# Kernel tuning notes

Measured on AMD Instinct MI355X. Metric: run time of the kernel, lower is better.

The kernel has to match this reference:

```python
import jax, jax.numpy as jnp
import numpy as np

# LightGCN propagation constants
N_USERS = 50000
N_ITEMS = 100000
N_NODES = N_USERS + N_ITEMS          # rows of the symmetric normalized adjacency
N_EDGES = 2400000                    # nnz of sparse adjacency (avg degree ~16)
LATENT_DIM = 64                      # config['latent_dim_rec']
N_LAYERS = 3                         # config['lightGCN_n_layers']
BATCH = 4096


def setup_inputs() -> dict:
    key = jax.random.key(0)
    ks = jax.random.split(key, 7)
    # Embedding tables, init std=0.1 as in nn.init.normal_(std=0.1)
    emb_user = 0.1 * jax.random.normal(ks[0], (N_USERS, LATENT_DIM), dtype=jnp.float32)
    emb_item = 0.1 * jax.random.normal(ks[1], (N_ITEMS, LATENT_DIM), dtype=jnp.float32)
    # Sparse normalized adjacency in COO form (fixed structure reused every layer)
    src = jax.random.randint(ks[2], (N_EDGES,), 0, N_NODES, dtype=jnp.int32)
    dst = jax.random.randint(ks[3], (N_EDGES,), 0, N_NODES, dtype=jnp.int32)
    # values ~ 1/sqrt(deg_i * deg_j) scale for avg degree 16
    vals = jax.random.uniform(ks[4], (N_EDGES,), dtype=jnp.float32) / 16.0
    users = jax.random.randint(ks[5], (BATCH,), 0, N_USERS, dtype=jnp.int32)
    items = jax.random.randint(ks[6], (BATCH,), 0, N_ITEMS, dtype=jnp.int32)
    return {"emb_user": emb_user, "emb_item": emb_item, "vals": vals,
            "src": src, "dst": dst, "users": users, "items": items}


def _spmm(vals, src, dst, x):
    # y[dst] += vals * x[src]  == torch.sparse.mm(G, x)
    return jax.ops.segment_sum(vals[:, None] * x[src], dst, num_segments=N_NODES)


def reference(emb_user, emb_item, vals, src, dst, users, items):
    # computer(): stack layer embeddings and mean-pool, fused as running sum
    all_emb = jnp.concatenate([emb_user, emb_item], axis=0)  # [N, D]
    acc = all_emb
    x = all_emb
    for _ in range(N_LAYERS):
        x = _spmm(vals, src, dst, x)
        acc = acc + x
    light_out = acc / jnp.asarray(N_LAYERS + 1, dtype=acc.dtype)
    users_emb = light_out[users]                 # [B, D]
    items_emb = light_out[N_USERS + items]       # [B, D]
    gamma = jnp.sum(users_emb * items_emb, axis=1)  # [B]
    return gamma
```

## Files before the change

### kernel.cpp

```cpp
#include <hip/hip_runtime.h>


#define N_USERS 50000
#define N_ITEMS 100000
#define N_NODES 150000
#define N_EDGES 2400000
#define DIM 64
#define BATCH 4096

#define CHUNKS 512
#define CHUNK_EDGES 4688
#define PPT 5
#define KB 256
#define NPB 586
#define ECAP 10240
#define GSTR 16
#define CONVB 2344

typedef unsigned int uint;
typedef float v2f __attribute__((ext_vector_type(2)));

__device__ __forceinline__ uint pack_bf16(float a, float b) {
    uint ua = __float_as_uint(a), ub = __float_as_uint(b);
    ua = (ua + 0x7FFFu + ((ua >> 16) & 1u)) >> 16;
    ub = (ub + 0x7FFFu + ((ub >> 16) & 1u)) >> 16;
    return ua | (ub << 16);
}

__device__ __forceinline__ v2f unpack_bf16x2(uint w) {
    v2f r;
    r.x = __uint_as_float(w << 16);
    r.y = __uint_as_float(w & 0xFFFF0000u);
    return r;
}

__global__ __launch_bounds__(1024) void part_kernel(
        const int* __restrict__ src, const int* __restrict__ dstA,
        const float* __restrict__ vals, int* __restrict__ gcur,
        int2* __restrict__ coarse,
        const float* __restrict__ emb_user, const float* __restrict__ emb_item,
        uint2* __restrict__ t0) {
    int t = threadIdx.x;
    if (blockIdx.x >= CHUNKS) {
        int i = (blockIdx.x - CHUNKS) * 1024 + t;
        if (i < N_NODES * DIM / 4) {
            const int userN4 = N_USERS * DIM / 4;
            float4 v;
            if (i < userN4) v = ((const float4*)emb_user)[i];
            else            v = ((const float4*)emb_item)[i - userN4];
            t0[i] = make_uint2(pack_bf16(v.x, v.y), pack_bf16(v.z, v.w));
        }
        return;
    }
    __shared__ int2 stage[CHUNK_EDGES];
    __shared__ unsigned char stage_b[CHUNK_EDGES];
    __shared__ int h[KB];
    __shared__ int hoff[KB];
    __shared__ int delta[KB];
    __shared__ int wsum4[4];
    int c = blockIdx.x;
    if (t < KB) h[t] = 0;
    __syncthreads();
    int base = c * CHUNK_EDGES;
    int ecnt = min(CHUNK_EDGES, N_EDGES - base);
    int d_c[PPT];
    int r_c[PPT];
#pragma unroll
    for (int u = 0; u < PPT; ++u) {
        int i = t + u * 1024;
        d_c[u] = 0;
        r_c[u] = 0;
        if (i < ecnt) {
            int d = dstA[base + i];
            d_c[u] = d;
            r_c[u] = atomicAdd(&h[(int)((unsigned)d / NPB)], 1);
        }
    }
    __syncthreads();
    int lane = t & 63, wid = t >> 6;
    if (t < KB) {
        int v = h[t];
        int incl = v;
#pragma unroll
        for (int o = 1; o < 64; o <<= 1) {
            int add = __shfl_up(incl, o, 64);
            if (lane >= o) incl += add;
        }
        hoff[t] = incl - v;
        if (lane == 63) wsum4[wid] = incl;
    }
    __syncthreads();
    if (t < 64) {
        int vv = (lane < 4) ? wsum4[lane] : 0;
        int inc2 = vv;
#pragma unroll
        for (int o = 1; o < 4; o <<= 1) {
            int add = __shfl_up(inc2, o, 64);
            if (lane >= o) inc2 += add;
        }
        if (lane < 4) wsum4[lane] = inc2 - vv;
    }
    __syncthreads();
    if (t < KB) {
        int off = hoff[t] + wsum4[t >> 6];
        hoff[t] = off;
        int cb = atomicAdd(&gcur[t * GSTR], h[t]);
        delta[t] = t * ECAP + cb - off;
    }
    __syncthreads();
#pragma unroll
    for (int u = 0; u < PPT; ++u) {
        int i = t + u * 1024;
        if (i < ecnt) {
            int e = base + i;
            int d = d_c[u];
            int b = (int)((unsigned)d / NPB);
            int dl = d - b * NPB;
            int pos = hoff[b] + r_c[u];
            stage[pos] = make_int2(src[e] | (dl << 18), __float_as_int(vals[e]));
            stage_b[pos] = (unsigned char)b;
        }
    }
    __syncthreads();
#pragma unroll
    for (int u = 0; u < PPT; ++u) {
        int j = t + u * 1024;
        if (j < ecnt) {
            int b = stage_b[j];
            int idx = j + delta[b];
            if (idx < (b + 1) * ECAP)
                coarse[idx] = stage[j];
        }
    }
}

__global__ __launch_bounds__(1024) void p4f_fine(int2* __restrict__ coarse,
                                                 const int* __restrict__ gcur,
                                                 uint* __restrict__ rowinfo) {
    __shared__ int2 eds[ECAP];
    __shared__ unsigned short iperm[ECAP];
    __shared__ int cnt[640];
    __shared__ int rs_[640];
    __shared__ int cur_[640];
    __shared__ int wsum[16];
    int k = blockIdx.x, t = threadIdx.x;
    int rbase = k * ECAP;
    int ne = min(gcur[k * GSTR], ECAP);
    for (int i = t; i < ne; i += 1024) eds[i] = coarse[rbase + i];
    if (t < 640) cnt[t] = 0;
    __syncthreads();
    for (int i = t; i < ne; i += 1024)
        atomicAdd(&cnt[eds[i].x >> 18], 1);
    __syncthreads();
    int wid = t >> 6, lane = t & 63;
    if (t < 640) {
        int v = cnt[t];
        int incl = v;
#pragma unroll
        for (int o = 1; o < 64; o <<= 1) {
            int add = __shfl_up(incl, o, 64);
            if (lane >= o) incl += add;
        }
        rs_[t] = incl - v;
        if (lane == 63) wsum[wid] = incl;
    }
    __syncthreads();
    if (t < 64) {
        int vv = (lane < 10) ? wsum[lane] : 0;
        int inc2 = vv;
#pragma unroll
        for (int o = 1; o < 16; o <<= 1) {
            int add = __shfl_up(inc2, o, 64);
            if (lane >= o) inc2 += add;
        }
        if (lane < 10) wsum[lane] = inc2 - vv;
    }
    __syncthreads();
    if (t < 640) rs_[t] += wsum[wid];
    __syncthreads();
    int nodes0 = k * NPB;
    int nb = min(NPB, N_NODES - nodes0);
    if (t < nb)
        rowinfo[nodes0 + t] = (uint)(rbase + rs_[t]) | ((uint)cnt[t] << 22);
    if (t < 640) cur_[t] = rs_[t];
    __syncthreads();
    for (int i = t; i < ne; i += 1024) {
        int dl = eds[i].x >> 18;
        int p = atomicAdd(&cur_[dl], 1);
        iperm[p] = (unsigned short)i;
    }
    __syncthreads();
    for (int j = t; j < ne; j += 1024) {
        int2 ev = eds[iperm[j]];
        coarse[rbase + j] = make_int2(ev.x & 0x3FFFF, ev.y);
    }
}

__global__ __launch_bounds__(256) void spmm_kernel(
        const uint* __restrict__ rowinfo, const int2* __restrict__ epair,
        const uint* __restrict__ xin, uint* __restrict__ xout) {
    int wave = (blockIdx.x * 256 + threadIdx.x) >> 6;
    int lane = threadIdx.x & 63;
    int g = lane >> 3;
    int l = lane & 7;
    int n = wave * 8 + g;
    bool live = n < N_NODES;
    uint ri = live ? rowinfo[n] : 0u;
    int s = (int)(ri & 0x3FFFFFu);
    int e = live ? s + (int)(ri >> 22) : s;
    int gbase = g * 8;
    v2f a0 = {0.f, 0.f}, a1 = {0.f, 0.f}, a2 = {0.f, 0.f}, a3 = {0.f, 0.f};
    for (int jb = s; jb < e; jb += 8) {
        int jl = jb + l;
        int2 ev = epair[jl < e ? jl : (e - 1)];
        float vw = (jl < e) ? __int_as_float(ev.y) : 0.f;
        int sx = ev.x;
        int srcs[8];
        float ws[8];
#pragma unroll
        for (int u = 0; u < 8; ++u) {
            srcs[u] = __shfl(sx, gbase + u, 64);
            ws[u]   = __shfl(vw, gbase + u, 64);
        }
        uint4 r[8];
#pragma unroll
        for (int u = 0; u < 8; ++u)
            r[u] = ((const uint4*)(xin + (size_t)srcs[u] * 32))[l];
#pragma unroll
        for (int u = 0; u < 8; ++u) {
            a0 += ws[u] * unpack_bf16x2(r[u].x);
            a1 += ws[u] * unpack_bf16x2(r[u].y);
            a2 += ws[u] * unpack_bf16x2(r[u].z);
            a3 += ws[u] * unpack_bf16x2(r[u].w);
        }
    }
    if (live) {
        uint4 o;
        o.x = pack_bf16(a0.x, a0.y);
        o.y = pack_bf16(a1.x, a1.y);
        o.z = pack_bf16(a2.x, a2.y);
        o.w = pack_bf16(a3.x, a3.y);
        ((uint4*)(xout + (size_t)n * 32))[l] = o;
    }
}

__global__ __launch_bounds__(256) void batch_row_kernel(
        const int* __restrict__ users, const int* __restrict__ items,
        const float* __restrict__ emb_user, const float* __restrict__ emb_item,
        const uint* __restrict__ x1, const uint* __restrict__ x2,
        const uint* __restrict__ rowinfo, const int2* __restrict__ epair,
        float4* __restrict__ rows) {
    int w = (blockIdx.x * 256 + threadIdx.x) >> 6;
    int lane = threadIdx.x & 63;
    int g = lane >> 4;
    int l = lane & 15;
    bool isU = w < BATCH;
    int b = isU ? w : w - BATCH;
    int idx = isU ? users[b] : items[b];
    int n = isU ? idx : N_USERS + idx;
    uint ri = rowinfo[n];
    int s = (int)(ri & 0x3FFFFFu);
    int e = s + (int)(ri >> 22);
    v2f a0 = {0.f, 0.f}, a1 = {0.f, 0.f};
    for (int j0 = s + g; j0 < e; j0 += 16) {
        int2 ev[4];
        float vv[4];
        uint2 rr[4];
#pragma unroll
        for (int u = 0; u < 4; ++u) {
            int j = j0 + 4 * u;
            bool p = (u == 0) || (j < e);
            ev[u] = epair[p ? j : j0];
            vv[u] = p ? __int_as_float(ev[u].y) : 0.f;
        }
#pragma unroll
        for (int u = 0; u < 4; ++u)
            rr[u] = ((const uint2*)(x2 + (size_t)ev[u].x * 32))[l];
#pragma unroll
        for (int u = 0; u < 4; ++u) {
            a0 += vv[u] * unpack_bf16x2(rr[u].x);
            a1 += vv[u] * unpack_bf16x2(rr[u].y);
        }
    }
#pragma unroll
    for (int off = 16; off < 64; off <<= 1) {
        a0.x += __shfl_xor(a0.x, off, 64);
        a0.y += __shfl_xor(a0.y, off, 64);
        a1.x += __shfl_xor(a1.x, off, 64);
        a1.y += __shfl_xor(a1.y, off, 64);
    }
    if (g == 0) {
        const float* t0row = isU ? (emb_user + (size_t)idx * DIM)
                                 : (emb_item + (size_t)idx * DIM);
        float4 x0 = ((const float4*)t0row)[l];
        uint2 w1 = ((const uint2*)(x1 + (size_t)n * 32))[l];
        uint2 w2 = ((const uint2*)(x2 + (size_t)n * 32))[l];
        v2f b10 = unpack_bf16x2(w1.x), b11 = unpack_bf16x2(w1.y);
        v2f b20 = unpack_bf16x2(w2.x), b21 = unpack_bf16x2(w2.y);
        float4 r;
        r.x = x0.x + b10.x + b20.x + a0.x;
        r.y = x0.y + b10.y + b20.y + a0.y;
        r.z = x0.z + b11.x + b21.x + a1.x;
        r.w = x0.w + b11.y + b21.y + a1.y;
        rows[(size_t)w * 16 + l] = r;
    }
}

__global__ __launch_bounds__(256) void dot_kernel(const float* __restrict__ rows,
                                                  float* __restrict__ out) {
    int t = blockIdx.x * 256 + threadIdx.x;
    int b = t >> 6;
    int lane = t & 63;
    float p = rows[(size_t)b * DIM + lane] * rows[(size_t)(BATCH + b) * DIM + lane];
#pragma unroll
    for (int o = 32; o > 0; o >>= 1) p += __shfl_down(p, o, 64);
    if (lane == 0) out[b] = p * (1.0f / 16.0f);
}

extern "C" void kernel_launch(void* const* d_in, const int* in_sizes, int n_in,
                              void* d_out, int out_size, void* d_ws, size_t ws_size,
                              hipStream_t stream) {
    const float* emb_user = (const float*)d_in[0];
    const float* emb_item = (const float*)d_in[1];
    const float* vals     = (const float*)d_in[2];
    const int*   src      = (const int*)d_in[3];
    const int*   dst      = (const int*)d_in[4];
    const int*   users    = (const int*)d_in[5];
    const int*   items    = (const int*)d_in[6];
    float* out = (float*)d_out;

    char* ws = (char*)d_ws;
    size_t off = 0;
    auto walloc = [&](size_t bytes) -> void* {
        void* p = ws + off;
        off += (bytes + 255) & ~(size_t)255;
        return p;
    };
    const size_t ROWB = (size_t)N_NODES * DIM * 2;
    uint* t0          = (uint*)walloc(ROWB);
    uint* x1          = (uint*)walloc(ROWB);
    uint* x2          = (uint*)walloc(ROWB);
    int2* coarse      = (int2*)walloc((size_t)KB * ECAP * 8);
    int*  gcur        = (int*) walloc((size_t)KB * GSTR * 4);
    uint* rowinfo     = (uint*)walloc((size_t)N_NODES * 4);
    float4* rows      = (float4*)walloc((size_t)2 * BATCH * DIM * 4);

    hipMemsetAsync(gcur, 0, (size_t)KB * GSTR * 4, stream);

    part_kernel<<<CHUNKS + CONVB, 1024, 0, stream>>>(
        src, dst, vals, gcur, coarse, emb_user, emb_item, (uint2*)t0);
    p4f_fine<<<KB, 1024, 0, stream>>>(coarse, gcur, rowinfo);

    const int SPMM_BLOCKS = (N_NODES / 8 * 64 + 255) / 256;
    spmm_kernel<<<SPMM_BLOCKS, 256, 0, stream>>>(rowinfo, coarse, t0, x1);
    spmm_kernel<<<SPMM_BLOCKS, 256, 0, stream>>>(rowinfo, coarse, x1, x2);
    batch_row_kernel<<<(2 * BATCH) / 4, 256, 0, stream>>>(
        users, items, emb_user, emb_item, x1, x2, rowinfo, coarse, rows);
    dot_kernel<<<(BATCH * 64) / 256, 256, 0, stream>>>((const float*)rows, out);
}
```

Before: 236.0 us.

## Fuse batch row gather with dot product and reuse counting atomics for bucketing

The final layer's per-row gather and the dot-product kernel become one kernel. Each wave handles one batch pair, user row in the lower half and item row in the upper half, and the halves are combined with cross-lane shuffles. This removes the intermediate rows buffer and one launch. Separately, the fine partition kernel keeps the atomicAdd return values from the counting pass as within-bucket offsets, which drops the second atomic pass and one barrier. The cost is that each row now gets half as many lanes for its edge loop, and the atomic results must sit in registers.

```diff
diff --git a/kernel.cpp b/kernel.cpp
--- a/kernel.cpp
+++ b/kernel.cpp
@@ -14,6 +14,7 @@
 #define KB 256
 #define NPB 586
 #define ECAP 10240
+#define MAXIT 10
 #define GSTR 16
 #define CONVB 2344
 
@@ -141,7 +142,6 @@
     __shared__ unsigned short iperm[ECAP];
     __shared__ int cnt[640];
     __shared__ int rs_[640];
-    __shared__ int cur_[640];
     __shared__ int wsum[16];
     int k = blockIdx.x, t = threadIdx.x;
     int rbase = k * ECAP;
@@ -149,8 +149,14 @@
     for (int i = t; i < ne; i += 1024) eds[i] = coarse[rbase + i];
     if (t < 640) cnt[t] = 0;
     __syncthreads();
-    for (int i = t; i < ne; i += 1024)
-        atomicAdd(&cnt[eds[i].x >> 18], 1);
+    int rr[MAXIT];
+#pragma unroll
+    for (int u = 0; u < MAXIT; ++u) {
+        int i = t + u * 1024;
+        rr[u] = 0;
+        if (i < ne)
+            rr[u] = atomicAdd(&cnt[eds[i].x >> 18], 1);
+    }
     __syncthreads();
     int wid = t >> 6, lane = t & 63;
     if (t < 640) {
@@ -182,12 +188,13 @@
     int nb = min(NPB, N_NODES - nodes0);
     if (t < nb)
         rowinfo[nodes0 + t] = (uint)(rbase + rs_[t]) | ((uint)cnt[t] << 22);
-    if (t < 640) cur_[t] = rs_[t];
-    __syncthreads();
-    for (int i = t; i < ne; i += 1024) {
-        int dl = eds[i].x >> 18;
-        int p = atomicAdd(&cur_[dl], 1);
-        iperm[p] = (unsigned short)i;
+#pragma unroll
+    for (int u = 0; u < MAXIT; ++u) {
+        int i = t + u * 1024;
+        if (i < ne) {
+            int dl = eds[i].x >> 18;
+            iperm[rs_[dl] + rr[u]] = (unsigned short)i;
+        }
     }
     __syncthreads();
     for (int j = t; j < ne; j += 1024) {
@@ -244,31 +251,30 @@
     }
 }
 
-__global__ __launch_bounds__(256) void batch_row_kernel(
+__global__ __launch_bounds__(256) void batch_dot_kernel(
         const int* __restrict__ users, const int* __restrict__ items,
         const float* __restrict__ emb_user, const float* __restrict__ emb_item,
         const uint* __restrict__ x1, const uint* __restrict__ x2,
         const uint* __restrict__ rowinfo, const int2* __restrict__ epair,
-        float4* __restrict__ rows) {
-    int w = (blockIdx.x * 256 + threadIdx.x) >> 6;
+        float* __restrict__ out) {
+    int b = (blockIdx.x * 256 + threadIdx.x) >> 6;
     int lane = threadIdx.x & 63;
-    int g = lane >> 4;
+    int hg = (lane >> 4) & 1;
     int l = lane & 15;
-    bool isU = w < BATCH;
-    int b = isU ? w : w - BATCH;
+    bool isU = lane < 32;
     int idx = isU ? users[b] : items[b];
     int n = isU ? idx : N_USERS + idx;
     uint ri = rowinfo[n];
     int s = (int)(ri & 0x3FFFFFu);
     int e = s + (int)(ri >> 22);
     v2f a0 = {0.f, 0.f}, a1 = {0.f, 0.f};
-    for (int j0 = s + g; j0 < e; j0 += 16) {
+    for (int j0 = s + hg; j0 < e; j0 += 8) {
         int2 ev[4];
         float vv[4];
         uint2 rr[4];
 #pragma unroll
         for (int u = 0; u < 4; ++u) {
-            int j = j0 + 4 * u;
+            int j = j0 + 2 * u;
             bool p = (u == 0) || (j < e);
             ev[u] = epair[p ? j : j0];
             vv[u] = p ? __int_as_float(ev[u].y) : 0.f;
@@ -282,38 +288,28 @@
             a1 += vv[u] * unpack_bf16x2(rr[u].y);
         }
     }
-#pragma unroll
-    for (int off = 16; off < 64; off <<= 1) {
-        a0.x += __shfl_xor(a0.x, off, 64);
-        a0.y += __shfl_xor(a0.y, off, 64);
-        a1.x += __shfl_xor(a1.x, off, 64);
-        a1.y += __shfl_xor(a1.y, off, 64);
-    }
-    if (g == 0) {
-        const float* t0row = isU ? (emb_user + (size_t)idx * DIM)
-                                 : (emb_item + (size_t)idx * DIM);
-        float4 x0 = ((const float4*)t0row)[l];
-        uint2 w1 = ((const uint2*)(x1 + (size_t)n * 32))[l];
-        uint2 w2 = ((const uint2*)(x2 + (size_t)n * 32))[l];
-        v2f b10 = unpack_bf16x2(w1.x), b11 = unpack_bf16x2(w1.y);
-        v2f b20 = unpack_bf16x2(w2.x), b21 = unpack_bf16x2(w2.y);
-        float4 r;
-        r.x = x0.x + b10.x + b20.x + a0.x;
-        r.y = x0.y + b10.y + b20.y + a0.y;
-        r.z = x0.z + b11.x + b21.x + a1.x;
-        r.w = x0.w + b11.y + b21.y + a1.y;
-        rows[(size_t)w * 16 + l] = r;
-    }
-}
-
-__global__ __launch_bounds__(256) void dot_kernel(const float* __restrict__ rows,
-                                                  float* __restrict__ out) {
-    int t = blockIdx.x * 256 + threadIdx.x;
-    int b = t >> 6;
-    int lane = t & 63;
-    float p = rows[(size_t)b * DIM + lane] * rows[(size_t)(BATCH + b) * DIM + lane];
-#pragma unroll
-    for (int o = 32; o > 0; o >>= 1) p += __shfl_down(p, o, 64);
+    a0.x += __shfl_xor(a0.x, 16, 64);
+    a0.y += __shfl_xor(a0.y, 16, 64);
+    a1.x += __shfl_xor(a1.x, 16, 64);
+    a1.y += __shfl_xor(a1.y, 16, 64);
+    const float* t0row = isU ? (emb_user + (size_t)idx * DIM)
+                             : (emb_item + (size_t)idx * DIM);
+    float4 x0 = ((const float4*)t0row)[l];
+    uint2 w1 = ((const uint2*)(x1 + (size_t)n * 32))[l];
+    uint2 w2 = ((const uint2*)(x2 + (size_t)n * 32))[l];
+    v2f b10 = unpack_bf16x2(w1.x), b11 = unpack_bf16x2(w1.y);
+    v2f b20 = unpack_bf16x2(w2.x), b21 = unpack_bf16x2(w2.y);
+    float rx = x0.x + b10.x + b20.x + a0.x;
+    float ry = x0.y + b10.y + b20.y + a0.y;
+    float rz = x0.z + b11.x + b21.x + a1.x;
+    float rw = x0.w + b11.y + b21.y + a1.y;
+    float ox = __shfl_xor(rx, 32, 64);
+    float oy = __shfl_xor(ry, 32, 64);
+    float oz = __shfl_xor(rz, 32, 64);
+    float ow = __shfl_xor(rw, 32, 64);
+    float p = rx * ox + ry * oy + rz * oz + rw * ow;
+#pragma unroll
+    for (int o = 1; o < 16; o <<= 1) p += __shfl_xor(p, o, 64);
     if (lane == 0) out[b] = p * (1.0f / 16.0f);
 }
 
@@ -343,7 +339,6 @@
     int2* coarse      = (int2*)walloc((size_t)KB * ECAP * 8);
     int*  gcur        = (int*) walloc((size_t)KB * GSTR * 4);
     uint* rowinfo     = (uint*)walloc((size_t)N_NODES * 4);
-    float4* rows      = (float4*)walloc((size_t)2 * BATCH * DIM * 4);
 
     hipMemsetAsync(gcur, 0, (size_t)KB * GSTR * 4, stream);
 
@@ -354,7 +349,6 @@
     const int SPMM_BLOCKS = (N_NODES / 8 * 64 + 255) / 256;
     spmm_kernel<<<SPMM_BLOCKS, 256, 0, stream>>>(rowinfo, coarse, t0, x1);
     spmm_kernel<<<SPMM_BLOCKS, 256, 0, stream>>>(rowinfo, coarse, x1, x2);
-    batch_row_kernel<<<(2 * BATCH) / 4, 256, 0, stream>>>(
-        users, items, emb_user, emb_item, x1, x2, rowinfo, coarse, rows);
-    dot_kernel<<<(BATCH * 64) / 256, 256, 0, stream>>>((const float*)rows, out);
-}
+    batch_dot_kernel<<<(BATCH * 64) / 256, 256, 0, stream>>>(
+        users, items, emb_user, emb_item, x1, x2, rowinfo, coarse, out);
+}
```

After: 235.9 us. No clear change (-0.1%).
